# Performance work log

Hardware: AMD Instinct MI355X
Metric: run time of the kernel (lower is better)

## Reference

```python
import jax, jax.numpy as jnp
import numpy as np

NUM_CLASSES = 19
IGNORE_INDEX = 255
FOCAL_GAMMA = 3.0
FOCAL_WEIGHT = 1.0
EPS = 1e-6


def setup_inputs() -> dict:
    key = jax.random.key(0)
    k1, k2 = jax.random.split(key)
    logits = jax.random.normal(k1, (8, NUM_CLASSES, 512, 512), dtype=jnp.float32)
    targets = jax.random.randint(k2, (8, 512, 512), 0, NUM_CLASSES, dtype=jnp.int64)
    return {"logits": logits, "targets": targets}


def reference(logits, targets):
    C = NUM_CLASSES
    # [B,C,H,W] -> [N,C] log-probs, N = B*H*W
    logp = jax.nn.log_softmax(logits, axis=1)
    lp = jnp.transpose(logp, (0, 2, 3, 1)).reshape(-1, C)
    t = targets.reshape(-1)
    valid = (t != IGNORE_INDEX)
    tc = jnp.clip(t, 0, C - 1)  # safe index for ignored pixels
    validf = valid.astype(lp.dtype)
    n_valid = jnp.maximum(jnp.sum(validf), 1.0)

    # mean cross entropy over valid pixels (F.cross_entropy with ignore_index)
    nll = -jnp.take_along_axis(lp, tc[:, None], axis=1)[:, 0]
    ce = jnp.sum(nll * validf) / n_valid

    # per-class focal term: -log(p_t) * (1 - p_t)^gamma, p_t clamped to [1e-6, 1]
    pt = jnp.clip(jnp.exp(-nll), EPS, 1.0)
    focal_terms = -jnp.log(pt) * (1.0 - pt) ** FOCAL_GAMMA

    # single-pass segment reduce: per-class sum and count over valid pixels
    sums = jax.ops.segment_sum(focal_terms * validf, tc, num_segments=C)
    counts = jax.ops.segment_sum(validf, tc, num_segments=C)
    present = counts > 0
    per_class_mean = sums / jnp.maximum(counts, 1.0)
    n_present = jnp.maximum(jnp.sum(present.astype(lp.dtype)), 1.0)
    focal = jnp.sum(jnp.where(present, per_class_mean, 0.0)) / n_present

    return ce + FOCAL_WEIGHT * focal
```

## Files before the change

kernel.cpp:

```cpp
#include <hip/hip_runtime.h>


#define NCLS 19
#define IGNORE_IDX 255
#define HW4 65536
#define FOCAL_EPS 1e-6f
#define NBLK 2048
#define NQ 40

typedef float f32x4 __attribute__((ext_vector_type(4)));
typedef int   i32x4 __attribute__((ext_vector_type(4)));

__global__ __launch_bounds__(256) void focal_main(
        const float* __restrict__ logits,
        const int*   __restrict__ targets,
        float* __restrict__ P) {
    __shared__ float    s_csum[NCLS];
    __shared__ unsigned s_ccnt[NCLS];
    __shared__ float    s_wnll[4];
    __shared__ int      s_wcnt[4];

    const int tid = threadIdx.x;
    if (tid < NCLS) { s_csum[tid] = 0.0f; s_ccnt[tid] = 0u; }
    __syncthreads();

    const unsigned g = blockIdx.x * 256u + tid;
    const unsigned b = g >> 16;
    const unsigned q = g & 65535u;
    const f32x4* base = reinterpret_cast<const f32x4*>(logits)
                        + (size_t)b * (NCLS * (size_t)HW4) + q;

    const i32x4 t4 = __builtin_nontemporal_load(
        reinterpret_cast<const i32x4*>(targets) + g);
    const int tt[4] = { t4.x, t4.y, t4.z, t4.w };
    int  tc[4];
    bool fv[4];
#pragma unroll
    for (int j = 0; j < 4; ++j) {
        tc[j] = min(max(tt[j], 0), NCLS - 1);
        fv[j] = (tt[j] != IGNORE_IDX);
    }

    float s[4]  = {0.0f, 0.0f, 0.0f, 0.0f};
    float xt[4] = {0.0f, 0.0f, 0.0f, 0.0f};
#pragma unroll
    for (int c = 0; c < NCLS; ++c) {
        const f32x4 v = __builtin_nontemporal_load(base + (size_t)c * HW4);
        const float vv[4] = { v.x, v.y, v.z, v.w };
#pragma unroll
        for (int j = 0; j < 4; ++j) {
            s[j] += __expf(vv[j]);
            if (c == tc[j]) xt[j] = vv[j];
        }
    }

    float nll_acc = 0.0f;
    int   vcnt    = 0;
#pragma unroll
    for (int j = 0; j < 4; ++j) {
        const float lse = __logf(s[j]);
        const float nll = lse - xt[j];
        float pt = __expf(-nll);
        pt = fminf(fmaxf(pt, FOCAL_EPS), 1.0f);
        const float om = 1.0f - pt;
        const float f  = -__logf(pt) * om * om * om;
        if (fv[j]) {
            nll_acc += nll; ++vcnt;
            atomicAdd(&s_csum[tc[j]], f);
            atomicAdd(&s_ccnt[tc[j]], 1u);
        }
    }

#pragma unroll
    for (int off = 32; off > 0; off >>= 1) {
        nll_acc += __shfl_down(nll_acc, off);
        vcnt    += __shfl_down(vcnt, off);
    }
    const int wid = tid >> 6, lane = tid & 63;
    if (lane == 0) { s_wnll[wid] = nll_acc; s_wcnt[wid] = vcnt; }
    __syncthreads();

    const unsigned bid = blockIdx.x;
    if (tid == 0) {
        float bn = s_wnll[0] + s_wnll[1] + s_wnll[2] + s_wnll[3];
        int   bc = s_wcnt[0] + s_wcnt[1] + s_wcnt[2] + s_wcnt[3];
        __builtin_nontemporal_store(bn,        &P[0 * NBLK + bid]);
        __builtin_nontemporal_store((float)bc, &P[1 * NBLK + bid]);
    }
    if (tid < NCLS) {
        __builtin_nontemporal_store(s_csum[tid],        &P[(2 + tid) * NBLK + bid]);
        __builtin_nontemporal_store((float)s_ccnt[tid], &P[(2 + NCLS + tid) * NBLK + bid]);
    }
}

__global__ __launch_bounds__(1024) void focal_final(
        const float* __restrict__ P, float* __restrict__ out) {
    __shared__ double s_q[NQ];
    const int tid  = threadIdx.x;
    const int wid  = tid >> 6;
    const int lane = tid & 63;

    for (int q = wid; q < NQ; q += 16) {
        double v = 0.0;
#pragma unroll
        for (int k = 0; k < NBLK / 64; ++k)
            v += (double)P[q * NBLK + lane + 64 * k];
#pragma unroll
        for (int off = 32; off > 0; off >>= 1)
            v += __shfl_down(v, off);
        if (lane == 0) s_q[q] = v;
    }
    __syncthreads();

    if (tid == 0) {
        double nv = s_q[1];
        if (nv < 1.0) nv = 1.0;
        const double ce = s_q[0] / nv;

        double fsum = 0.0, npres = 0.0;
        for (int c = 0; c < NCLS; ++c) {
            const double cnt = s_q[2 + NCLS + c];
            if (cnt > 0.0) {
                fsum += s_q[2 + c] / (cnt < 1.0 ? 1.0 : cnt);
                npres += 1.0;
            }
        }
        if (npres < 1.0) npres = 1.0;
        out[0] = (float)(ce + fsum / npres);
    }
}

extern "C" void kernel_launch(void* const* d_in, const int* in_sizes, int n_in,
                              void* d_out, int out_size, void* d_ws, size_t ws_size,
                              hipStream_t stream) {
    const float* logits  = (const float*)d_in[0];
    const int*   targets = (const int*)d_in[1];
    float*       out     = (float*)d_out;
    float*       P       = (float*)d_ws;

    focal_main<<<NBLK, 256, 0, stream>>>(logits, targets, P);
    focal_final<<<1, 1024, 0, stream>>>(P, out);
}
```

Before: 231.1 us.

## Fuse final reduction into main kernel via last-block atomic counter

Drops the separate single-block finalize kernel. Each block now writes its partials with system-coherent stores and bumps a global atomic counter, and the last block to finish does the cross-block reduction using vectorized coherent loads. This removes one kernel launch and its serialization gap, but adds a memset launch and a per-block fence and atomic. The nontemporal load hints on the logits and targets are also removed, which can change how the streaming reads interact with the cache.

```diff
diff --git a/kernel.cpp b/kernel.cpp
--- a/kernel.cpp
+++ b/kernel.cpp
@@ -7,18 +7,28 @@
 #define FOCAL_EPS 1e-6f
 #define NBLK 2048
 #define NQ 40
+#define CTR_OFF (NQ * NBLK * sizeof(float))
 
 typedef float f32x4 __attribute__((ext_vector_type(4)));
 typedef int   i32x4 __attribute__((ext_vector_type(4)));
 
+__device__ __forceinline__ void store_sc(float* p, float v) {
+    asm volatile("global_store_dword %0, %1, off sc0 sc1"
+                 :: "v"(p), "v"(v) : "memory");
+}
+
 __global__ __launch_bounds__(256) void focal_main(
         const float* __restrict__ logits,
         const int*   __restrict__ targets,
-        float* __restrict__ P) {
+        float* __restrict__ P,
+        unsigned* __restrict__ ctr,
+        float* __restrict__ out) {
     __shared__ float    s_csum[NCLS];
     __shared__ unsigned s_ccnt[NCLS];
     __shared__ float    s_wnll[4];
     __shared__ int      s_wcnt[4];
+    __shared__ double   s_q[NQ];
+    __shared__ int      s_last;
 
     const int tid = threadIdx.x;
     if (tid < NCLS) { s_csum[tid] = 0.0f; s_ccnt[tid] = 0u; }
@@ -30,8 +40,7 @@
     const f32x4* base = reinterpret_cast<const f32x4*>(logits)
                         + (size_t)b * (NCLS * (size_t)HW4) + q;
 
-    const i32x4 t4 = __builtin_nontemporal_load(
-        reinterpret_cast<const i32x4*>(targets) + g);
+    const i32x4 t4 = *(reinterpret_cast<const i32x4*>(targets) + g);
     const int tt[4] = { t4.x, t4.y, t4.z, t4.w };
     int  tc[4];
     bool fv[4];
@@ -45,7 +54,7 @@
     float xt[4] = {0.0f, 0.0f, 0.0f, 0.0f};
 #pragma unroll
     for (int c = 0; c < NCLS; ++c) {
-        const f32x4 v = __builtin_nontemporal_load(base + (size_t)c * HW4);
+        const f32x4 v = base[(size_t)c * HW4];
         const float vv[4] = { v.x, v.y, v.z, v.w };
 #pragma unroll
         for (int j = 0; j < 4; ++j) {
@@ -84,31 +93,43 @@
     if (tid == 0) {
         float bn = s_wnll[0] + s_wnll[1] + s_wnll[2] + s_wnll[3];
         int   bc = s_wcnt[0] + s_wcnt[1] + s_wcnt[2] + s_wcnt[3];
-        __builtin_nontemporal_store(bn,        &P[0 * NBLK + bid]);
-        __builtin_nontemporal_store((float)bc, &P[1 * NBLK + bid]);
+        store_sc(&P[0 * NBLK + bid], bn);
+        store_sc(&P[1 * NBLK + bid], (float)bc);
     }
     if (tid < NCLS) {
-        __builtin_nontemporal_store(s_csum[tid],        &P[(2 + tid) * NBLK + bid]);
-        __builtin_nontemporal_store((float)s_ccnt[tid], &P[(2 + NCLS + tid) * NBLK + bid]);
+        store_sc(&P[(2 + tid) * NBLK + bid],        s_csum[tid]);
+        store_sc(&P[(2 + NCLS + tid) * NBLK + bid], (float)s_ccnt[tid]);
     }
-}
+    asm volatile("s_waitcnt vmcnt(0)" ::: "memory");
+    __syncthreads();
 
-__global__ __launch_bounds__(1024) void focal_final(
-        const float* __restrict__ P, float* __restrict__ out) {
-    __shared__ double s_q[NQ];
-    const int tid  = threadIdx.x;
-    const int wid  = tid >> 6;
-    const int lane = tid & 63;
+    if (tid == 0) {
+        const unsigned old = atomicAdd(ctr, 1u);
+        s_last = (old == NBLK - 1u);
+    }
+    __syncthreads();
+    if (!s_last) return;
 
-    for (int q = wid; q < NQ; q += 16) {
+    for (int qq = wid * 10; qq < wid * 10 + 10 && qq < NQ; ++qq) {
+        const float* qbase = P + (size_t)qq * NBLK + 4 * lane;
+        f32x4 vb[8];
+#pragma unroll
+        for (int k = 0; k < 8; ++k) {
+            const f32x4* p = reinterpret_cast<const f32x4*>(qbase + 256 * k);
+            asm volatile("global_load_dwordx4 %0, %1, off sc0 sc1"
+                         : "=v"(vb[k]) : "v"(p));
+        }
+        asm volatile("s_waitcnt vmcnt(0)" ::: "memory");
+        __builtin_amdgcn_sched_barrier(0);
         double v = 0.0;
 #pragma unroll
-        for (int k = 0; k < NBLK / 64; ++k)
-            v += (double)P[q * NBLK + lane + 64 * k];
+        for (int k = 0; k < 8; ++k)
+            v += (double)vb[k].x + (double)vb[k].y
+               + (double)vb[k].z + (double)vb[k].w;
 #pragma unroll
         for (int off = 32; off > 0; off >>= 1)
             v += __shfl_down(v, off);
-        if (lane == 0) s_q[q] = v;
+        if (lane == 0) s_q[qq] = v;
     }
     __syncthreads();
 
@@ -137,7 +158,8 @@
     const int*   targets = (const int*)d_in[1];
     float*       out     = (float*)d_out;
     float*       P       = (float*)d_ws;
+    unsigned*    ctr     = (unsigned*)((char*)d_ws + CTR_OFF);
 
-    focal_main<<<NBLK, 256, 0, stream>>>(logits, targets, P);
-    focal_final<<<1, 1024, 0, stream>>>(P, out);
+    hipMemsetAsync(ctr, 0, sizeof(unsigned), stream);
+    focal_main<<<NBLK, 256, 0, stream>>>(logits, targets, P, ctr, out);
 }
```

Measured after the change: 235.3 us. About the same (+1.8%).
